# Kernel tuning notes

Hardware: AMD Instinct MI355X
Metric: run time of the kernel (lower is better)

## Reference

```python
import jax, jax.numpy as jnp
import numpy as np

B, S, D, F, E = 8, 8192, 256, 1024, 8
ROUTE_KEY = 42  # fixed seed replacing torch's Categorical(...).sample()


def setup_inputs() -> dict:
    key = jax.random.key(0)
    ks = jax.random.split(key, 8)
    scale = 0.02
    return {
        "x": jax.random.normal(ks[0], (B, S, D), dtype=jnp.float32),
        "gate_w": jax.random.normal(ks[1], (D, E), dtype=jnp.float32) * scale,
        "gate_b": jnp.zeros((E,), dtype=jnp.float32),
        "w1": jax.random.normal(ks[2], (E, D, F), dtype=jnp.float32) * scale,
        "b1": jnp.zeros((E, F), dtype=jnp.float32),
        "w2": jax.random.normal(ks[3], (E, F, D), dtype=jnp.float32) * scale,
        "b2": jnp.zeros((E, D), dtype=jnp.float32),
    }


def reference(x, gate_w, gate_b, w1, b1, w2, b2):
    # Gate: logits -> softmax -> sample one expert per token.
    # (softmax is monotonic-preserving for categorical sampling, so sampling
    # from logits directly matches Categorical(softmax(logits)).sample().)
    gate_logits = jnp.einsum("bsd,de->bse", x, gate_w) + gate_b
    chosen = jax.random.categorical(jax.random.key(ROUTE_KEY), gate_logits)  # [B,S] int

    num_experts = w1.shape[0]
    out = jnp.zeros_like(x)
    for e in range(num_experts):  # small fixed expert count
        h = jax.nn.relu(jnp.einsum("bsd,df->bsf", x, w1[e]) + b1[e])
        y = jnp.einsum("bsf,fd->bsd", h, w2[e]) + b2[e]
        # scatter-write rows routed to expert e (dropout is identity in eval)
        out = out + jnp.where((chosen == e)[..., None], y, jnp.zeros((), x.dtype))
    return out
```

## Files before the change

kernel.cpp:

```cpp
#include <hip/hip_runtime.h>
#include <hip/hip_bf16.h>

#define NTOK 65536
#define DD 256
#define FF 1024
#define EE 8
#define BSTRIDE 12288
#define MTILE 128
#define NTILES (BSTRIDE / MTILE)
#define CHUNK_US 16384

typedef short bh8 __attribute__((ext_vector_type(8)));
typedef float f16v __attribute__((ext_vector_type(16)));

__device__ __forceinline__ unsigned rotl32(unsigned v, int d) {
  return (v << d) | (v >> (32 - d));
}

__device__ __forceinline__ unsigned jax_random_bits32(unsigned c0, unsigned c1) {
  const unsigned k0 = 0u, k1 = 42u;
  const unsigned k2 = 0x1BD11BDAu ^ k0 ^ k1;
  unsigned x0 = c0 + k0, x1 = c1 + k1;
#define TFR(r) { x0 += x1; x1 = rotl32(x1, (r)); x1 ^= x0; }
  TFR(13) TFR(15) TFR(26) TFR(6)
  x0 += k1; x1 += k2 + 1u;
  TFR(17) TFR(29) TFR(16) TFR(24)
  x0 += k2; x1 += k0 + 2u;
  TFR(13) TFR(15) TFR(26) TFR(6)
  x0 += k0; x1 += k1 + 3u;
  TFR(17) TFR(29) TFR(16) TFR(24)
  x0 += k1; x1 += k2 + 4u;
  TFR(13) TFR(15) TFR(26) TFR(6)
  x0 += k2; x1 += k0 + 5u;
#undef TFR
  return x0 ^ x1;
}

__device__ __forceinline__ ushort f2bf(float f) {
  union { float f; unsigned u; } c; c.f = f;
  unsigned r = c.u + 0x7fffu + ((c.u >> 16) & 1u);
  return (ushort)(r >> 16);
}

__global__ __launch_bounds__(1024) void gate_route3(
    const float* __restrict__ x, const float* __restrict__ gw,
    const float* __restrict__ gb, int* __restrict__ counts,
    int* __restrict__ buckets, ushort* __restrict__ xbf) {
  __shared__ float gwt[EE * DD];
  __shared__ int hist[EE], sbase[EE];
  __shared__ unsigned char chs[64];
  __shared__ short lps[64];

  const int tid = threadIdx.x;
  if (tid < EE) hist[tid] = 0;
  for (int i = tid; i < DD * EE; i += 1024) {
    const int d = i >> 3, e = i & 7;
    gwt[e * DD + d] = gw[i];
  }
  __syncthreads();

  const int lane = tid & 63;
  const int wave = tid >> 6;
  const int grp = lane >> 4;
  const int gl = lane & 15;
  const int slot = wave * 4 + grp;
  const int t = blockIdx.x * 64 + slot;

  float acc[EE] = {0.f, 0.f, 0.f, 0.f, 0.f, 0.f, 0.f, 0.f};
  const float* xr = x + (size_t)t * DD;
#pragma unroll
  for (int j = 0; j < 4; ++j) {
    const int d0 = j * 64 + gl * 4;
    const float4 xv = *reinterpret_cast<const float4*>(xr + d0);
    if (xbf != nullptr) {
      ushort4 xb;
      xb.x = f2bf(xv.x); xb.y = f2bf(xv.y); xb.z = f2bf(xv.z); xb.w = f2bf(xv.w);
      *reinterpret_cast<ushort4*>(xbf + (size_t)t * DD + d0) = xb;
    }
#pragma unroll
    for (int e = 0; e < EE; ++e) {
      const float4 g = *reinterpret_cast<const float4*>(&gwt[e * DD + d0]);
      acc[e] = fmaf(xv.x, g.x, acc[e]);
      acc[e] = fmaf(xv.y, g.y, acc[e]);
      acc[e] = fmaf(xv.z, g.z, acc[e]);
      acc[e] = fmaf(xv.w, g.w, acc[e]);
    }
  }
#pragma unroll
  for (int off = 8; off >= 1; off >>= 1)
#pragma unroll
    for (int e = 0; e < EE; ++e) acc[e] += __shfl_xor(acc[e], off);

  const int e = gl & 7;
  float logit = 0.f;
#pragma unroll
  for (int q = 0; q < EE; ++q) logit = (e == q) ? acc[q] : logit;
  logit += gb[e];

  const unsigned bits = jax_random_bits32(0u, (unsigned)(t * EE + e));
  const float f = __uint_as_float((bits >> 9) | 0x3f800000u) - 1.0f;
  const float u = fmaxf(1.17549435e-38f, f);
  float val = -logf(-logf(u)) + logit;
  int idx = e;
#pragma unroll
  for (int off = 4; off > 0; off >>= 1) {
    const float ov = __shfl_xor(val, off);
    const int oi = __shfl_xor(idx, off);
    if (ov > val || (ov == val && oi < idx)) { val = ov; idx = oi; }
  }
  if (gl == 0) {
    const int lp = atomicAdd(&hist[idx], 1);
    chs[slot] = (unsigned char)idx;
    lps[slot] = (short)lp;
  }
  __syncthreads();
  if (tid < EE) sbase[tid] = atomicAdd(&counts[tid], hist[tid]);
  __syncthreads();
  if (tid < 64) {
    const int ee = chs[tid];
    const int p = sbase[ee] + lps[tid];
    if (p < BSTRIDE) buckets[ee * BSTRIDE + p] = blockIdx.x * 64 + tid;
  }
}

__global__ __launch_bounds__(256) void prep_w1s(
    const float* __restrict__ w1, ushort* __restrict__ w1s) {
  __shared__ float ts[64][65];
  const int e = blockIdx.z;
  const int f0 = blockIdx.x * 64, d0 = blockIdx.y * 64;
  const int tx = threadIdx.x, ty = threadIdx.y;
  const float* s = w1 + (size_t)e * DD * FF;
  char* dimg = (char*)(w1s + (size_t)e * 16 * CHUNK_US + blockIdx.x * CHUNK_US);
#pragma unroll
  for (int i = 0; i < 16; ++i)
    ts[ty * 16 + i][tx] = s[(size_t)(d0 + ty * 16 + i) * FF + f0 + tx];
  __syncthreads();
#pragma unroll
  for (int i = 0; i < 16; ++i) {
    const int fl = ty * 16 + i;
    const int byte = ((fl * 512 + (d0 + tx) * 2)) ^ ((fl & 31) << 4);
    *reinterpret_cast<ushort*>(dimg + byte) = f2bf(ts[tx][fl]);
  }
}

__global__ __launch_bounds__(256) void prep_w2s(
    const float* __restrict__ w2, ushort* __restrict__ w2s) {
  __shared__ float ts[64][65];
  const int e = blockIdx.z;
  const int d0 = blockIdx.x * 64, f0 = blockIdx.y * 64;
  const int tx = threadIdx.x, ty = threadIdx.y;
  const float* s = w2 + (size_t)e * FF * DD;
  char* dimg = (char*)(w2s + (size_t)e * 16 * CHUNK_US + blockIdx.y * CHUNK_US);
#pragma unroll
  for (int i = 0; i < 16; ++i)
    ts[ty * 16 + i][tx] = s[(size_t)(f0 + ty * 16 + i) * DD + d0 + tx];
  __syncthreads();
#pragma unroll
  for (int i = 0; i < 16; ++i) {
    const int d = d0 + ty * 16 + i;
    const int byte = ((d * 128 + tx * 2)) ^ ((d & 7) << 4);
    *reinterpret_cast<ushort*>(dimg + byte) = f2bf(ts[tx][ty * 16 + i]);
  }
}

__device__ __forceinline__ void stage32k(const ushort* g, ushort* l, int wid, int lane) {
  const ushort* gs = g + wid * 2048 + lane * 8;
  ushort* ls = l + wid * 2048;
#pragma unroll
  for (int i = 0; i < 4; ++i)
    __builtin_amdgcn_global_load_lds(
        (const __attribute__((address_space(1))) void*)(gs + i * 512),
        (__attribute__((address_space(3))) void*)(ls + i * 512), 16, 0, 0);
}

__global__ __launch_bounds__(512, 2) void ffn_mfma5(
    const ushort* __restrict__ xbf, const ushort* __restrict__ w1s,
    const float* __restrict__ b1, const ushort* __restrict__ w2s,
    const float* __restrict__ b2, const int* __restrict__ counts,
    const int* __restrict__ buckets, float* __restrict__ out) {
  const int e = blockIdx.x & 7;
  const int tile = blockIdx.x >> 3;
  const int cnt = min(counts[e], BSTRIDE);
  const int m0 = tile * MTILE;
  if (m0 >= cnt) return;

  __shared__ ushort W1b[CHUNK_US];
  __shared__ ushort W2b[CHUNK_US];
  __shared__ ushort Hb[MTILE * 64];
  __shared__ int toks[MTILE];

  const int tid = threadIdx.x;
  const int lane = tid & 63;
  const int wid = tid >> 6;
  const int l31 = lane & 31;
  const int h = lane >> 5;

  const int g = wid >> 2;
  const int j = wid & 3;
  const int mh = wid >> 2;
  const int dq = wid & 3;

  if (tid < MTILE) {
    const int i = m0 + tid;
    toks[tid] = buckets[e * BSTRIDE + (i < cnt ? i : cnt - 1)];
  }

  const ushort* w1g = w1s + (size_t)e * 16 * CHUNK_US;
  const ushort* w2g = w2s + (size_t)e * 16 * CHUNK_US;

  stage32k(w1g, W1b, wid, lane);
  stage32k(w2g, W2b, wid, lane);

  const int mx = m0 + j * 32 + l31;
  const int tokx = buckets[e * BSTRIDE + (mx < cnt ? mx : cnt - 1)];
  const ushort* xp = xbf + (size_t)tokx * DD + h * 8;
  bh8 xf[16];
#pragma unroll
  for (int ks = 0; ks < 16; ++ks)
    xf[ks] = *reinterpret_cast<const bh8*>(xp + ks * 16);

  const int fl = g * 32 + l31;
  const int w1x = (fl & 31) << 4;
  const int mrow = j * 32 + l31;
  const int hswz = (mrow & 7) << 4;

  __syncthreads();

  f16v yacc[2][2] = {};

#pragma unroll 1
  for (int c = 0; c < 16; ++c) {
    {
      const char* wb = reinterpret_cast<const char*>(W1b);
      f16v hacc = {};
#pragma unroll
      for (int ks = 0; ks < 16; ++ks) {
        const int byte = (fl * 512 + ks * 32 + h * 16) ^ w1x;
        const bh8 a = *reinterpret_cast<const bh8*>(wb + byte);
        hacc = __builtin_amdgcn_mfma_f32_32x32x16_bf16(a, xf[ks], hacc, 0, 0, 0);
      }
      char* hbase = reinterpret_cast<char*>(Hb);
#pragma unroll
      for (int q = 0; q < 4; ++q) {
        const float4 b1v = *reinterpret_cast<const float4*>(
            b1 + e * FF + c * 64 + g * 32 + q * 8 + 4 * h);
        ushort4 hv;
        hv.x = f2bf(fmaxf(hacc[q * 4 + 0] + b1v.x, 0.f));
        hv.y = f2bf(fmaxf(hacc[q * 4 + 1] + b1v.y, 0.f));
        hv.z = f2bf(fmaxf(hacc[q * 4 + 2] + b1v.z, 0.f));
        hv.w = f2bf(fmaxf(hacc[q * 4 + 3] + b1v.w, 0.f));
        const int byte = (mrow * 128 + (g * 32 + q * 8 + 4 * h) * 2) ^ hswz;
        *reinterpret_cast<ushort4*>(hbase + byte) = hv;
      }
    }
    __syncthreads();

    if (c < 15)
      stage32k(w1g + (size_t)(c + 1) * CHUNK_US, W1b, wid, lane);

    {
      const char* hbase = reinterpret_cast<const char*>(Hb);
      const char* wb = reinterpret_cast<const char*>(W2b);
      const int d0 = dq * 64 + l31;
#pragma unroll
      for (int ks = 0; ks < 4; ++ks) {
        bh8 hfa[2];
#pragma unroll
        for (int mb = 0; mb < 2; ++mb) {
          const int m = mh * 64 + mb * 32 + l31;
          const int byte = (m * 128 + ks * 32 + h * 16) ^ ((m & 7) << 4);
          hfa[mb] = *reinterpret_cast<const bh8*>(hbase + byte);
        }
        const int b0 = (d0 * 128 + ks * 32 + h * 16) ^ ((d0 & 7) << 4);
        const int d1 = d0 + 32;
        const int b1y = (d1 * 128 + ks * 32 + h * 16) ^ ((d1 & 7) << 4);
        const bh8 bf0 = *reinterpret_cast<const bh8*>(wb + b0);
        const bh8 bf1 = *reinterpret_cast<const bh8*>(wb + b1y);
        yacc[0][0] = __builtin_amdgcn_mfma_f32_32x32x16_bf16(hfa[0], bf0, yacc[0][0], 0, 0, 0);
        yacc[0][1] = __builtin_amdgcn_mfma_f32_32x32x16_bf16(hfa[0], bf1, yacc[0][1], 0, 0, 0);
        yacc[1][0] = __builtin_amdgcn_mfma_f32_32x32x16_bf16(hfa[1], bf0, yacc[1][0], 0, 0, 0);
        yacc[1][1] = __builtin_amdgcn_mfma_f32_32x32x16_bf16(hfa[1], bf1, yacc[1][1], 0, 0, 0);
      }
    }
    __syncthreads();

    if (c < 15)
      stage32k(w2g + (size_t)(c + 1) * CHUNK_US, W2b, wid, lane);
  }

  const float b2v0 = b2[e * DD + dq * 64 + l31];
  const float b2v1 = b2[e * DD + dq * 64 + 32 + l31];
#pragma unroll
  for (int mb = 0; mb < 2; ++mb) {
#pragma unroll
    for (int r = 0; r < 16; ++r) {
      const int m = mh * 64 + mb * 32 + (r & 3) + 8 * (r >> 2) + 4 * h;
      if (m0 + m < cnt) {
        const size_t ro = (size_t)toks[m] * DD + dq * 64 + l31;
        out[ro] = yacc[mb][0][r] + b2v0;
        out[ro + 32] = yacc[mb][1][r] + b2v1;
      }
    }
  }
}

__global__ __launch_bounds__(512) void ffn_fp32(
    const float* __restrict__ x, const float* __restrict__ w1,
    const float* __restrict__ b1, const float* __restrict__ w2,
    const float* __restrict__ b2, const int* __restrict__ counts,
    const int* __restrict__ buckets, float* __restrict__ out, int bstride) {
  const int e = blockIdx.y;
  const int cnt = min(counts[e], bstride);
  const int m0 = blockIdx.x * 64;
  if (m0 >= cnt) return;

  __shared__ float Xt[DD][64];
  __shared__ float Ht[64][64];
  __shared__ int toks[64];

  const int tid = threadIdx.x;
  if (tid < 64) {
    const int i = m0 + tid;
    toks[tid] = buckets[e * bstride + (i < cnt ? i : cnt - 1)];
  }
  __syncthreads();

  for (int idx = tid; idx < 64 * (DD / 4); idx += 512) {
    const int r = idx >> 6;
    const int c4 = idx & 63;
    const float4 v = *reinterpret_cast<const float4*>(x + (size_t)toks[r] * DD + c4 * 4);
    Xt[c4 * 4 + 0][r] = v.x;
    Xt[c4 * 4 + 1][r] = v.y;
    Xt[c4 * 4 + 2][r] = v.z;
    Xt[c4 * 4 + 3][r] = v.w;
  }
  __syncthreads();

  const int fg = tid & 15;
  const int mg = tid >> 4;
  const int dc = tid & 63;
  const int mgrp = tid >> 6;

  float yacc[8][4];
#pragma unroll
  for (int i = 0; i < 8; ++i)
#pragma unroll
    for (int jj = 0; jj < 4; ++jj) yacc[i][jj] = 0.f;

  for (int fc0 = 0; fc0 < FF; fc0 += 64) {
    float hacc[2][4];
#pragma unroll
    for (int i = 0; i < 2; ++i)
#pragma unroll
      for (int jj = 0; jj < 4; ++jj) hacc[i][jj] = 0.f;

    const float* w1p = w1 + (size_t)e * DD * FF + fc0 + fg * 4;
    for (int d = 0; d < DD; ++d) {
      const float4 w = *reinterpret_cast<const float4*>(w1p + (size_t)d * FF);
      const float2 xv = *reinterpret_cast<const float2*>(&Xt[d][mg * 2]);
      const float ws[4] = {w.x, w.y, w.z, w.w};
      const float xl[2] = {xv.x, xv.y};
#pragma unroll
      for (int i = 0; i < 2; ++i)
#pragma unroll
        for (int jj = 0; jj < 4; ++jj)
          hacc[i][jj] = fmaf(xl[i], ws[jj], hacc[i][jj]);
    }
#pragma unroll
    for (int jj = 0; jj < 4; ++jj) {
      const float bb = b1[e * FF + fc0 + fg * 4 + jj];
      Ht[fg * 4 + jj][mg * 2 + 0] = fmaxf(hacc[0][jj] + bb, 0.f);
      Ht[fg * 4 + jj][mg * 2 + 1] = fmaxf(hacc[1][jj] + bb, 0.f);
    }
    __syncthreads();

    const float* w2p = w2 + (size_t)e * FF * DD + (size_t)fc0 * DD + dc * 4;
    for (int f = 0; f < 64; ++f) {
      const float4 w = *reinterpret_cast<const float4*>(w2p + (size_t)f * DD);
      const float4 h0 = *reinterpret_cast<const float4*>(&Ht[f][mgrp * 8]);
      const float4 h1 = *reinterpret_cast<const float4*>(&Ht[f][mgrp * 8 + 4]);
      const float hs[8] = {h0.x, h0.y, h0.z, h0.w, h1.x, h1.y, h1.z, h1.w};
      const float ws[4] = {w.x, w.y, w.z, w.w};
#pragma unroll
      for (int i = 0; i < 8; ++i)
#pragma unroll
        for (int jj = 0; jj < 4; ++jj)
          yacc[i][jj] = fmaf(hs[i], ws[jj], yacc[i][jj]);
    }
    __syncthreads();
  }

#pragma unroll
  for (int i = 0; i < 8; ++i) {
    const int r = mgrp * 8 + i;
    if (m0 + r < cnt) {
      float4 o;
      o.x = yacc[i][0] + b2[e * DD + dc * 4 + 0];
      o.y = yacc[i][1] + b2[e * DD + dc * 4 + 1];
      o.z = yacc[i][2] + b2[e * DD + dc * 4 + 2];
      o.w = yacc[i][3] + b2[e * DD + dc * 4 + 3];
      *reinterpret_cast<float4*>(out + (size_t)toks[r] * DD + dc * 4) = o;
    }
  }
}

extern "C" void kernel_launch(void* const* d_in, const int* in_sizes, int n_in,
                              void* d_out, int out_size, void* d_ws, size_t ws_size,
                              hipStream_t stream) {
  const float* x  = (const float*)d_in[0];
  const float* gw = (const float*)d_in[1];
  const float* gb = (const float*)d_in[2];
  const float* w1 = (const float*)d_in[3];
  const float* b1 = (const float*)d_in[4];
  const float* w2 = (const float*)d_in[5];
  const float* b2 = (const float*)d_in[6];
  float* out = (float*)d_out;

  int* counts = (int*)d_ws;
  int* buckets = (int*)((char*)d_ws + 4096);
  ushort* w1s = (ushort*)((char*)d_ws + 524288);
  ushort* w2s = (ushort*)((char*)d_ws + 524288 + 4194304);
  ushort* xbf = (ushort*)((char*)d_ws + 524288 + 2ull * 4194304);
  const size_t need = 524288 + 2ull * 4194304 + (size_t)NTOK * DD * 2;

  hipMemsetAsync(d_ws, 0, 4096, stream);

  if (ws_size >= need) {
    hipLaunchKernelGGL(gate_route3, dim3(NTOK / 64), dim3(1024), 0, stream,
                       x, gw, gb, counts, buckets, xbf);
    hipLaunchKernelGGL(prep_w1s, dim3(FF / 64, DD / 64, EE), dim3(64, 4), 0, stream,
                       w1, w1s);
    hipLaunchKernelGGL(prep_w2s, dim3(DD / 64, FF / 64, EE), dim3(64, 4), 0, stream,
                       w2, w2s);
    hipLaunchKernelGGL(ffn_mfma5, dim3(NTILES * EE), dim3(512), 0, stream,
                       xbf, w1s, b1, w2s, b2, counts, buckets, out);
  } else {
    hipLaunchKernelGGL(gate_route3, dim3(NTOK / 64), dim3(1024), 0, stream,
                       x, gw, gb, counts, buckets, (ushort*)nullptr);
    hipLaunchKernelGGL(ffn_fp32, dim3(NTOK / 64, EE), dim3(512), 0, stream,
                       x, w1, b1, w2, b2, counts, buckets, out, BSTRIDE);
  }
}
```

Before: 175.4 us.

## Halve FFN block to 4 waves with larger per-wave tiles and register-packed H

Rewrites the expert FFN kernel to use 256 threads, with each wave computing two 32-row M tiles in GEMM1 and a 64x128 output tile in GEMM2. Each LDS weight fragment is now reused across more MFMAs. H is written to LDS directly in MFMA A-operand layout, using cross-half-wave shuffles to pack bf16 pairs, so GEMM2 reads it as contiguous lane vectors. The W2 swizzle is widened to 32 rows and the staging routine loads twice as much per wave. Token indices are now read from global memory in the epilogue instead of a shared array. The trade-offs are fewer waves per CU for hiding latency and higher register pressure from 8 accumulators.

After: 364.4 us. +107.8%, slower.

```diff
diff --git a/kernel.cpp b/kernel.cpp
--- a/kernel.cpp
+++ b/kernel.cpp
@@ -42,6 +42,10 @@
   return (ushort)(r >> 16);
 }
 
+__device__ __forceinline__ unsigned pack2(float a, float b) {
+  return (unsigned)f2bf(a) | ((unsigned)f2bf(b) << 16);
+}
+
 __global__ __launch_bounds__(1024) void gate_route3(
     const float* __restrict__ x, const float* __restrict__ gw,
     const float* __restrict__ gb, int* __restrict__ counts,
@@ -158,22 +162,22 @@
 #pragma unroll
   for (int i = 0; i < 16; ++i) {
     const int d = d0 + ty * 16 + i;
-    const int byte = ((d * 128 + tx * 2)) ^ ((d & 7) << 4);
+    const int byte = ((d * 128 + tx * 2)) ^ ((d & 31) << 4);
     *reinterpret_cast<ushort*>(dimg + byte) = f2bf(ts[tx][ty * 16 + i]);
   }
 }
 
-__device__ __forceinline__ void stage32k(const ushort* g, ushort* l, int wid, int lane) {
-  const ushort* gs = g + wid * 2048 + lane * 8;
-  ushort* ls = l + wid * 2048;
-#pragma unroll
-  for (int i = 0; i < 4; ++i)
+__device__ __forceinline__ void stage32k4(const ushort* g, ushort* l, int wid, int lane) {
+  const ushort* gs = g + wid * 4096 + lane * 8;
+  ushort* ls = l + wid * 4096;
+#pragma unroll
+  for (int i = 0; i < 8; ++i)
     __builtin_amdgcn_global_load_lds(
         (const __attribute__((address_space(1))) void*)(gs + i * 512),
         (__attribute__((address_space(3))) void*)(ls + i * 512), 16, 0, 0);
 }
 
-__global__ __launch_bounds__(512, 2) void ffn_mfma5(
+__global__ __launch_bounds__(256, 2) void ffn_mfma6(
     const ushort* __restrict__ xbf, const ushort* __restrict__ w1s,
     const float* __restrict__ b1, const ushort* __restrict__ w2s,
     const float* __restrict__ b2, const int* __restrict__ counts,
@@ -186,119 +190,126 @@
 
   __shared__ ushort W1b[CHUNK_US];
   __shared__ ushort W2b[CHUNK_US];
-  __shared__ ushort Hb[MTILE * 64];
-  __shared__ int toks[MTILE];
+  __shared__ ushort Hb[8192];
 
   const int tid = threadIdx.x;
   const int lane = tid & 63;
   const int wid = tid >> 6;
   const int l31 = lane & 31;
   const int h = lane >> 5;
-
-  const int g = wid >> 2;
-  const int j = wid & 3;
-  const int mh = wid >> 2;
-  const int dq = wid & 3;
-
-  if (tid < MTILE) {
-    const int i = m0 + tid;
-    toks[tid] = buckets[e * BSTRIDE + (i < cnt ? i : cnt - 1)];
-  }
+  const int g = wid & 1;
+  const int j = wid >> 1;
 
   const ushort* w1g = w1s + (size_t)e * 16 * CHUNK_US;
   const ushort* w2g = w2s + (size_t)e * 16 * CHUNK_US;
 
-  stage32k(w1g, W1b, wid, lane);
-  stage32k(w2g, W2b, wid, lane);
-
-  const int mx = m0 + j * 32 + l31;
-  const int tokx = buckets[e * BSTRIDE + (mx < cnt ? mx : cnt - 1)];
-  const ushort* xp = xbf + (size_t)tokx * DD + h * 8;
-  bh8 xf[16];
-#pragma unroll
-  for (int ks = 0; ks < 16; ++ks)
-    xf[ks] = *reinterpret_cast<const bh8*>(xp + ks * 16);
+  stage32k4(w1g, W1b, wid, lane);
+  stage32k4(w2g, W2b, wid, lane);
+
+  bh8 xf[2][16];
+#pragma unroll
+  for (int t = 0; t < 2; ++t) {
+    const int m = m0 + j * 64 + t * 32 + l31;
+    const int tok = buckets[e * BSTRIDE + (m < cnt ? m : cnt - 1)];
+    const ushort* xp = xbf + (size_t)tok * DD + h * 8;
+#pragma unroll
+    for (int ks = 0; ks < 16; ++ks)
+      xf[t][ks] = *reinterpret_cast<const bh8*>(xp + ks * 16);
+  }
 
   const int fl = g * 32 + l31;
   const int w1x = (fl & 31) << 4;
-  const int mrow = j * 32 + l31;
-  const int hswz = (mrow & 7) << 4;
-
-  __syncthreads();
-
-  f16v yacc[2][2] = {};
+  __syncthreads();
+
+  f16v yacc[2][4] = {};
 
 #pragma unroll 1
   for (int c = 0; c < 16; ++c) {
     {
       const char* wb = reinterpret_cast<const char*>(W1b);
-      f16v hacc = {};
+      f16v h0 = {}, h1 = {};
 #pragma unroll
       for (int ks = 0; ks < 16; ++ks) {
         const int byte = (fl * 512 + ks * 32 + h * 16) ^ w1x;
         const bh8 a = *reinterpret_cast<const bh8*>(wb + byte);
-        hacc = __builtin_amdgcn_mfma_f32_32x32x16_bf16(a, xf[ks], hacc, 0, 0, 0);
+        h0 = __builtin_amdgcn_mfma_f32_32x32x16_bf16(a, xf[0][ks], h0, 0, 0, 0);
+        h1 = __builtin_amdgcn_mfma_f32_32x32x16_bf16(a, xf[1][ks], h1, 0, 0, 0);
       }
-      char* hbase = reinterpret_cast<char*>(Hb);
-#pragma unroll
-      for (int q = 0; q < 4; ++q) {
-        const float4 b1v = *reinterpret_cast<const float4*>(
-            b1 + e * FF + c * 64 + g * 32 + q * 8 + 4 * h);
-        ushort4 hv;
-        hv.x = f2bf(fmaxf(hacc[q * 4 + 0] + b1v.x, 0.f));
-        hv.y = f2bf(fmaxf(hacc[q * 4 + 1] + b1v.y, 0.f));
-        hv.z = f2bf(fmaxf(hacc[q * 4 + 2] + b1v.z, 0.f));
-        hv.w = f2bf(fmaxf(hacc[q * 4 + 3] + b1v.w, 0.f));
-        const int byte = (mrow * 128 + (g * 32 + q * 8 + 4 * h) * 2) ^ hswz;
-        *reinterpret_cast<ushort4*>(hbase + byte) = hv;
+      char* hbb = reinterpret_cast<char*>(Hb);
+#pragma unroll
+      for (int t = 0; t < 2; ++t) {
+        const f16v& ha = t ? h1 : h0;
+        float hv[16];
+#pragma unroll
+        for (int q = 0; q < 4; ++q) {
+          const float4 bv = *reinterpret_cast<const float4*>(
+              b1 + e * FF + c * 64 + g * 32 + q * 8 + 4 * h);
+          hv[q * 4 + 0] = fmaxf(ha[q * 4 + 0] + bv.x, 0.f);
+          hv[q * 4 + 1] = fmaxf(ha[q * 4 + 1] + bv.y, 0.f);
+          hv[q * 4 + 2] = fmaxf(ha[q * 4 + 2] + bv.z, 0.f);
+          hv[q * 4 + 3] = fmaxf(ha[q * 4 + 3] + bv.w, 0.f);
+        }
+#pragma unroll
+        for (int ksl = 0; ksl < 2; ++ksl) {
+          const unsigned plo0 = pack2(hv[8 * ksl + 0], hv[8 * ksl + 1]);
+          const unsigned plo1 = pack2(hv[8 * ksl + 2], hv[8 * ksl + 3]);
+          const unsigned phi0 = pack2(hv[8 * ksl + 4], hv[8 * ksl + 5]);
+          const unsigned phi1 = pack2(hv[8 * ksl + 6], hv[8 * ksl + 7]);
+          const unsigned r0 = (unsigned)__shfl_xor((int)(h ? plo0 : phi0), 32);
+          const unsigned r1 = (unsigned)__shfl_xor((int)(h ? plo1 : phi1), 32);
+          uint4 w;
+          w.x = h ? r0 : plo0;
+          w.y = h ? r1 : plo1;
+          w.z = h ? phi0 : r0;
+          w.w = h ? phi1 : r1;
+          const int M = j * 2 + t, K = g * 2 + ksl;
+          *reinterpret_cast<uint4*>(hbb + (M * 4 + K) * 1024 + lane * 16) = w;
+        }
       }
     }
     __syncthreads();
 
     if (c < 15)
-      stage32k(w1g + (size_t)(c + 1) * CHUNK_US, W1b, wid, lane);
+      stage32k4(w1g + (size_t)(c + 1) * CHUNK_US, W1b, wid, lane);
 
     {
-      const char* hbase = reinterpret_cast<const char*>(Hb);
+      const char* hbb = reinterpret_cast<const char*>(Hb);
       const char* wb = reinterpret_cast<const char*>(W2b);
-      const int d0 = dq * 64 + l31;
-#pragma unroll
-      for (int ks = 0; ks < 4; ++ks) {
-        bh8 hfa[2];
-#pragma unroll
-        for (int mb = 0; mb < 2; ++mb) {
-          const int m = mh * 64 + mb * 32 + l31;
-          const int byte = (m * 128 + ks * 32 + h * 16) ^ ((m & 7) << 4);
-          hfa[mb] = *reinterpret_cast<const bh8*>(hbase + byte);
+#pragma unroll
+      for (int K = 0; K < 4; ++K) {
+        const bh8 a0 = *reinterpret_cast<const bh8*>(
+            hbb + ((j * 2 + 0) * 4 + K) * 1024 + lane * 16);
+        const bh8 a1 = *reinterpret_cast<const bh8*>(
+            hbb + ((j * 2 + 1) * 4 + K) * 1024 + lane * 16);
+#pragma unroll
+        for (int dt = 0; dt < 4; ++dt) {
+          const int d = g * 128 + dt * 32 + l31;
+          const int byte = (d * 128 + K * 32 + h * 16) ^ ((d & 31) << 4);
+          const bh8 b = *reinterpret_cast<const bh8*>(wb + byte);
+          yacc[0][dt] = __builtin_amdgcn_mfma_f32_32x32x16_bf16(a0, b, yacc[0][dt], 0, 0, 0);
+          yacc[1][dt] = __builtin_amdgcn_mfma_f32_32x32x16_bf16(a1, b, yacc[1][dt], 0, 0, 0);
         }
-        const int b0 = (d0 * 128 + ks * 32 + h * 16) ^ ((d0 & 7) << 4);
-        const int d1 = d0 + 32;
-        const int b1y = (d1 * 128 + ks * 32 + h * 16) ^ ((d1 & 7) << 4);
-        const bh8 bf0 = *reinterpret_cast<const bh8*>(wb + b0);
-        const bh8 bf1 = *reinterpret_cast<const bh8*>(wb + b1y);
-        yacc[0][0] = __builtin_amdgcn_mfma_f32_32x32x16_bf16(hfa[0], bf0, yacc[0][0], 0, 0, 0);
-        yacc[0][1] = __builtin_amdgcn_mfma_f32_32x32x16_bf16(hfa[0], bf1, yacc[0][1], 0, 0, 0);
-        yacc[1][0] = __builtin_amdgcn_mfma_f32_32x32x16_bf16(hfa[1], bf0, yacc[1][0], 0, 0, 0);
-        yacc[1][1] = __builtin_amdgcn_mfma_f32_32x32x16_bf16(hfa[1], bf1, yacc[1][1], 0, 0, 0);
       }
     }
     __syncthreads();
 
     if (c < 15)
-      stage32k(w2g + (size_t)(c + 1) * CHUNK_US, W2b, wid, lane);
-  }
-
-  const float b2v0 = b2[e * DD + dq * 64 + l31];
-  const float b2v1 = b2[e * DD + dq * 64 + 32 + l31];
-#pragma unroll
-  for (int mb = 0; mb < 2; ++mb) {
-#pragma unroll
-    for (int r = 0; r < 16; ++r) {
-      const int m = mh * 64 + mb * 32 + (r & 3) + 8 * (r >> 2) + 4 * h;
-      if (m0 + m < cnt) {
-        const size_t ro = (size_t)toks[m] * DD + dq * 64 + l31;
-        out[ro] = yacc[mb][0][r] + b2v0;
-        out[ro + 32] = yacc[mb][1][r] + b2v1;
+      stage32k4(w2g + (size_t)(c + 1) * CHUNK_US, W2b, wid, lane);
+  }
+
+#pragma unroll
+  for (int t = 0; t < 2; ++t) {
+#pragma unroll
+    for (int dt = 0; dt < 4; ++dt) {
+      const int d = g * 128 + dt * 32 + l31;
+      const float b2v = b2[e * DD + d];
+#pragma unroll
+      for (int r = 0; r < 16; ++r) {
+        const int m = j * 64 + t * 32 + (r & 3) + 8 * (r >> 2) + 4 * h;
+        if (m0 + m < cnt) {
+          const int tok = buckets[e * BSTRIDE + m0 + m];
+          out[(size_t)tok * DD + d] = yacc[t][dt][r] + b2v;
+        }
       }
     }
   }
@@ -432,7 +443,7 @@
                        w1, w1s);
     hipLaunchKernelGGL(prep_w2s, dim3(DD / 64, FF / 64, EE), dim3(64, 4), 0, stream,
                        w2, w2s);
-    hipLaunchKernelGGL(ffn_mfma5, dim3(NTILES * EE), dim3(512), 0, stream,
+    hipLaunchKernelGGL(ffn_mfma6, dim3(NTILES * EE), dim3(256), 0, stream,
                        xbf, w1s, b1, w2s, b2, counts, buckets, out);
   } else {
     hipLaunchKernelGGL(gate_route3, dim3(NTOK / 64), dim3(1024), 0, stream,
```

## Switch expert FFN to 16x16x32 MFMA with 64-row tiles and higher occupancy

Applied to the files above, without the earlier changes.

Rewrites the fused expert FFN kernel to process 64-token tiles using 16x16x32 bf16 MFMA instead of 32x32x16 on 128-token tiles. It shrinks the accumulator register footprint so four blocks per CU can be targeted, changes the H staging layout in shared memory into a fragment-ordered form, and widens the W2 swizzle to 32 rows. The aim is more resident waves to hide the per-chunk weight staging and barrier latency. The cost is that each block now reloads the full expert weights for half as many tokens, which doubles weight traffic from L2.

Result: faster. 168.0 us (-4.2%).

```diff
diff --git a/kernel.cpp b/kernel.cpp
--- a/kernel.cpp
+++ b/kernel.cpp
@@ -6,12 +6,12 @@
 #define FF 1024
 #define EE 8
 #define BSTRIDE 12288
-#define MTILE 128
+#define MTILE 64
 #define NTILES (BSTRIDE / MTILE)
 #define CHUNK_US 16384
 
 typedef short bh8 __attribute__((ext_vector_type(8)));
-typedef float f16v __attribute__((ext_vector_type(16)));
+typedef float f4v __attribute__((ext_vector_type(4)));
 
 __device__ __forceinline__ unsigned rotl32(unsigned v, int d) {
   return (v << d) | (v >> (32 - d));
@@ -42,6 +42,10 @@
   return (ushort)(r >> 16);
 }
 
+__device__ __forceinline__ unsigned pack2(float a, float b) {
+  return (unsigned)f2bf(a) | ((unsigned)f2bf(b) << 16);
+}
+
 __global__ __launch_bounds__(1024) void gate_route3(
     const float* __restrict__ x, const float* __restrict__ gw,
     const float* __restrict__ gb, int* __restrict__ counts,
@@ -158,7 +162,7 @@
 #pragma unroll
   for (int i = 0; i < 16; ++i) {
     const int d = d0 + ty * 16 + i;
-    const int byte = ((d * 128 + tx * 2)) ^ ((d & 7) << 4);
+    const int byte = ((d * 128 + tx * 2)) ^ ((d & 31) << 4);
     *reinterpret_cast<ushort*>(dimg + byte) = f2bf(ts[tx][ty * 16 + i]);
   }
 }
@@ -173,7 +177,7 @@
         (__attribute__((address_space(3))) void*)(ls + i * 512), 16, 0, 0);
 }
 
-__global__ __launch_bounds__(512, 2) void ffn_mfma5(
+__global__ __launch_bounds__(512, 4) void ffn_mfma10(
     const ushort* __restrict__ xbf, const ushort* __restrict__ w1s,
     const float* __restrict__ b1, const ushort* __restrict__ w2s,
     const float* __restrict__ b2, const int* __restrict__ counts,
@@ -186,24 +190,16 @@
 
   __shared__ ushort W1b[CHUNK_US];
   __shared__ ushort W2b[CHUNK_US];
-  __shared__ ushort Hb[MTILE * 64];
-  __shared__ int toks[MTILE];
+  __shared__ ushort Hb[4096];
 
   const int tid = threadIdx.x;
   const int lane = tid & 63;
   const int wid = tid >> 6;
-  const int l31 = lane & 31;
-  const int h = lane >> 5;
-
-  const int g = wid >> 2;
-  const int j = wid & 3;
-  const int mh = wid >> 2;
-  const int dq = wid & 3;
-
-  if (tid < MTILE) {
-    const int i = m0 + tid;
-    toks[tid] = buckets[e * BSTRIDE + (i < cnt ? i : cnt - 1)];
-  }
+  const int l15 = lane & 15;
+  const int q = lane >> 4;
+  const int fp = wid >> 2;
+  const int mt = wid & 3;
+  const int dh = wid >> 2;
 
   const ushort* w1g = w1s + (size_t)e * 16 * CHUNK_US;
   const ushort* w2g = w2s + (size_t)e * 16 * CHUNK_US;
@@ -211,46 +207,50 @@
   stage32k(w1g, W1b, wid, lane);
   stage32k(w2g, W2b, wid, lane);
 
-  const int mx = m0 + j * 32 + l31;
-  const int tokx = buckets[e * BSTRIDE + (mx < cnt ? mx : cnt - 1)];
-  const ushort* xp = xbf + (size_t)tokx * DD + h * 8;
-  bh8 xf[16];
-#pragma unroll
-  for (int ks = 0; ks < 16; ++ks)
-    xf[ks] = *reinterpret_cast<const bh8*>(xp + ks * 16);
-
-  const int fl = g * 32 + l31;
-  const int w1x = (fl & 31) << 4;
-  const int mrow = j * 32 + l31;
-  const int hswz = (mrow & 7) << 4;
-
-  __syncthreads();
-
-  f16v yacc[2][2] = {};
+  const int mxi = m0 + mt * 16 + l15;
+  const int tokx = buckets[e * BSTRIDE + (mxi < cnt ? mxi : cnt - 1)];
+  const ushort* xp = xbf + (size_t)tokx * DD + q * 8;
+  bh8 xf[8];
+#pragma unroll
+  for (int dks = 0; dks < 8; ++dks)
+    xf[dks] = *reinterpret_cast<const bh8*>(xp + dks * 32);
+
+  __syncthreads();
+
+  f4v yacc[8] = {};
 
 #pragma unroll 1
   for (int c = 0; c < 16; ++c) {
     {
       const char* wb = reinterpret_cast<const char*>(W1b);
-      f16v hacc = {};
-#pragma unroll
-      for (int ks = 0; ks < 16; ++ks) {
-        const int byte = (fl * 512 + ks * 32 + h * 16) ^ w1x;
-        const bh8 a = *reinterpret_cast<const bh8*>(wb + byte);
-        hacc = __builtin_amdgcn_mfma_f32_32x32x16_bf16(a, xf[ks], hacc, 0, 0, 0);
+      f4v h0 = {}, h1 = {};
+      const int fl0 = (2 * fp) * 16 + l15;
+      const int fl1 = (2 * fp + 1) * 16 + l15;
+#pragma unroll
+      for (int dks = 0; dks < 8; ++dks) {
+        const int co = (32 * dks + 8 * q) * 2;
+        const bh8 a0 = *reinterpret_cast<const bh8*>(
+            wb + ((fl0 * 512 + co) ^ ((fl0 & 31) << 4)));
+        const bh8 a1 = *reinterpret_cast<const bh8*>(
+            wb + ((fl1 * 512 + co) ^ ((fl1 & 31) << 4)));
+        h0 = __builtin_amdgcn_mfma_f32_16x16x32_bf16(a0, xf[dks], h0, 0, 0, 0);
+        h1 = __builtin_amdgcn_mfma_f32_16x16x32_bf16(a1, xf[dks], h1, 0, 0, 0);
       }
-      char* hbase = reinterpret_cast<char*>(Hb);
-#pragma unroll
-      for (int q = 0; q < 4; ++q) {
-        const float4 b1v = *reinterpret_cast<const float4*>(
-            b1 + e * FF + c * 64 + g * 32 + q * 8 + 4 * h);
-        ushort4 hv;
-        hv.x = f2bf(fmaxf(hacc[q * 4 + 0] + b1v.x, 0.f));
-        hv.y = f2bf(fmaxf(hacc[q * 4 + 1] + b1v.y, 0.f));
-        hv.z = f2bf(fmaxf(hacc[q * 4 + 2] + b1v.z, 0.f));
-        hv.w = f2bf(fmaxf(hacc[q * 4 + 3] + b1v.w, 0.f));
-        const int byte = (mrow * 128 + (g * 32 + q * 8 + 4 * h) * 2) ^ hswz;
-        *reinterpret_cast<ushort4*>(hbase + byte) = hv;
+      char* hbb = reinterpret_cast<char*>(Hb);
+#pragma unroll
+      for (int th = 0; th < 2; ++th) {
+        const int t = 2 * fp + th;
+        const float4 bv = *reinterpret_cast<const float4*>(
+            b1 + e * FF + c * 64 + t * 16 + 4 * q);
+        const f4v& ha = th ? h1 : h0;
+        const float v0 = fmaxf(ha[0] + bv.x, 0.f);
+        const float v1 = fmaxf(ha[1] + bv.y, 0.f);
+        const float v2 = fmaxf(ha[2] + bv.z, 0.f);
+        const float v3 = fmaxf(ha[3] + bv.w, 0.f);
+        const int laneT = (2 * th + (q >> 1)) * 16 + l15;
+        const int base = ((mt * 2 + fp) * 64 + laneT) * 16;
+        *reinterpret_cast<unsigned*>(hbb + base + (((2 * q + 0) & 3) << 2)) = pack2(v0, v1);
+        *reinterpret_cast<unsigned*>(hbb + base + (((2 * q + 1) & 3) << 2)) = pack2(v2, v3);
       }
     }
     __syncthreads();
@@ -259,27 +259,20 @@
       stage32k(w1g + (size_t)(c + 1) * CHUNK_US, W1b, wid, lane);
 
     {
-      const char* hbase = reinterpret_cast<const char*>(Hb);
+      const char* hbb = reinterpret_cast<const char*>(Hb);
       const char* wb = reinterpret_cast<const char*>(W2b);
-      const int d0 = dq * 64 + l31;
-#pragma unroll
-      for (int ks = 0; ks < 4; ++ks) {
-        bh8 hfa[2];
-#pragma unroll
-        for (int mb = 0; mb < 2; ++mb) {
-          const int m = mh * 64 + mb * 32 + l31;
-          const int byte = (m * 128 + ks * 32 + h * 16) ^ ((m & 7) << 4);
-          hfa[mb] = *reinterpret_cast<const bh8*>(hbase + byte);
+#pragma unroll
+      for (int ks = 0; ks < 2; ++ks) {
+        const bh8 af = *reinterpret_cast<const bh8*>(
+            hbb + ((mt * 2 + ks) * 64 + lane) * 16);
+        const int co = (32 * ks + 8 * q) * 2;
+#pragma unroll
+        for (int dt = 0; dt < 8; ++dt) {
+          const int d = (dh * 8 + dt) * 16 + l15;
+          const bh8 b = *reinterpret_cast<const bh8*>(
+              wb + ((d * 128 + co) ^ ((d & 31) << 4)));
+          yacc[dt] = __builtin_amdgcn_mfma_f32_16x16x32_bf16(af, b, yacc[dt], 0, 0, 0);
         }
-        const int b0 = (d0 * 128 + ks * 32 + h * 16) ^ ((d0 & 7) << 4);
-        const int d1 = d0 + 32;
-        const int b1y = (d1 * 128 + ks * 32 + h * 16) ^ ((d1 & 7) << 4);
-        const bh8 bf0 = *reinterpret_cast<const bh8*>(wb + b0);
-        const bh8 bf1 = *reinterpret_cast<const bh8*>(wb + b1y);
-        yacc[0][0] = __builtin_amdgcn_mfma_f32_32x32x16_bf16(hfa[0], bf0, yacc[0][0], 0, 0, 0);
-        yacc[0][1] = __builtin_amdgcn_mfma_f32_32x32x16_bf16(hfa[0], bf1, yacc[0][1], 0, 0, 0);
-        yacc[1][0] = __builtin_amdgcn_mfma_f32_32x32x16_bf16(hfa[1], bf0, yacc[1][0], 0, 0, 0);
-        yacc[1][1] = __builtin_amdgcn_mfma_f32_32x32x16_bf16(hfa[1], bf1, yacc[1][1], 0, 0, 0);
       }
     }
     __syncthreads();
@@ -288,18 +281,21 @@
       stage32k(w2g + (size_t)(c + 1) * CHUNK_US, W2b, wid, lane);
   }
 
-  const float b2v0 = b2[e * DD + dq * 64 + l31];
-  const float b2v1 = b2[e * DD + dq * 64 + 32 + l31];
-#pragma unroll
-  for (int mb = 0; mb < 2; ++mb) {
-#pragma unroll
-    for (int r = 0; r < 16; ++r) {
-      const int m = mh * 64 + mb * 32 + (r & 3) + 8 * (r >> 2) + 4 * h;
-      if (m0 + m < cnt) {
-        const size_t ro = (size_t)toks[m] * DD + dq * 64 + l31;
-        out[ro] = yacc[mb][0][r] + b2v0;
-        out[ro + 32] = yacc[mb][1][r] + b2v1;
-      }
+  int toks4[4];
+#pragma unroll
+  for (int r = 0; r < 4; ++r) {
+    const int m = m0 + mt * 16 + 4 * q + r;
+    toks4[r] = buckets[e * BSTRIDE + (m < cnt ? m : cnt - 1)];
+  }
+#pragma unroll
+  for (int dt = 0; dt < 8; ++dt) {
+    const int d = (dh * 8 + dt) * 16 + l15;
+    const float b2v = b2[e * DD + d];
+#pragma unroll
+    for (int r = 0; r < 4; ++r) {
+      const int m = mt * 16 + 4 * q + r;
+      if (m0 + m < cnt)
+        out[(size_t)toks4[r] * DD + d] = yacc[dt][r] + b2v;
     }
   }
 }
@@ -432,7 +428,7 @@
                        w1, w1s);
     hipLaunchKernelGGL(prep_w2s, dim3(DD / 64, FF / 64, EE), dim3(64, 4), 0, stream,
                        w2, w2s);
-    hipLaunchKernelGGL(ffn_mfma5, dim3(NTILES * EE), dim3(512), 0, stream,
+    hipLaunchKernelGGL(ffn_mfma10, dim3(NTILES * EE), dim3(512), 0, stream,
                        xbf, w1s, b1, w2s, b2, counts, buckets, out);
   } else {
     hipLaunchKernelGGL(gate_route3, dim3(NTOK / 64), dim3(1024), 0, stream,
```
